# Optimization experiments

Measured on AMD Instinct MI355X. Metric: run time of the kernel, lower is better.

The kernel has to match this reference:

```python
import jax, jax.numpy as jnp
import numpy as np

B, S, C, H = 2, 3144, 256, 8
HD = C // H                      # head_dim = key_dim = 32
SCALE = HD ** -0.5
QN = 8                           # queriesNum hard-coded in source
KS = 5                           # lepe depthwise conv kernel


def setup_inputs() -> dict:
    key = jax.random.key(0)
    ks = jax.random.split(key, 10)
    gain_qkv = 2 ** (-2.5) * (2.0 / (C + C)) ** 0.5  # xavier_normal std with gain 2^-2.5
    gain_out = (2.0 / (C + C)) ** 0.5
    return {
        "x": jax.random.normal(ks[0], (B, S, C), jnp.float32),
        "mask": jax.random.uniform(ks[1], (B, S, S), jnp.float32),
        "wq": jax.random.normal(ks[2], (C, C), jnp.float32) * gain_qkv,
        "bq": jnp.zeros((C,), jnp.float32),
        "wk": jax.random.normal(ks[3], (C, C), jnp.float32) * gain_qkv,
        "bk": jnp.zeros((C,), jnp.float32),
        "wv": jax.random.normal(ks[4], (C, C), jnp.float32) * gain_qkv,
        "bv": jnp.zeros((C,), jnp.float32),
        "lepe_w": jax.random.normal(ks[5], (KS, KS, 1, C), jnp.float32) * 0.05,  # depthwise HWIO
        "lepe_b": jnp.zeros((C,), jnp.float32),
        "wo": jax.random.normal(ks[6], (C, C), jnp.float32) * gain_out,
        "bo": jnp.zeros((C,), jnp.float32),
        "h": 56,
        "w": 56,
    }


def _dwconv(x_nhwc, kern, bias):
    # depthwise 5x5, stride 1, padding 2 (groups = channels)
    y = jax.lax.conv_general_dilated(
        x_nhwc, kern, window_strides=(1, 1), padding=((2, 2), (2, 2)),
        dimension_numbers=("NHWC", "HWIO", "NHWC"),
        feature_group_count=x_nhwc.shape[-1])
    return y + bias


def reference(x, mask, wq, bq, wk, bk, wv, bv, lepe_w, lepe_b, wo, bo, h, w):
    b, s, c = x.shape
    q = x @ wq.T + bq
    k = (x @ wk.T + bk) * SCALE
    v = x @ wv.T + bv
    # lepe positional residual on the non-query tokens
    lepe = _dwconv(v[:, QN:].reshape(b, h, w, c), lepe_w, lepe_b).reshape(b, h * w, c)
    qh = q.reshape(b, s, H, HD).transpose(0, 2, 1, 3)   # (b, H, s, hd)
    kh = k.reshape(b, s, H, HD).transpose(0, 2, 1, 3)
    vh = kh  # faithful to source: v_h = k.reshape(...)  (scaled k used as values)
    qk = jnp.einsum("bhqd,bhkd->bhqk", qh, kh)
    qk = qk + jnp.log(mask[:, None] + 1e-6)              # isSoftMask=True path
    attn = jax.nn.softmax(qk, axis=-1)
    out = jnp.einsum("bhqk,bhkd->bhqd", attn, vh)
    out = out.transpose(0, 2, 1, 3).reshape(b, s, c)
    out = out.at[:, QN:].add(lepe)
    return out @ wo.T + bo
```

## Files before the change

### kernel.cpp

```cpp
#include <hip/hip_runtime.h>


#define S_LEN 3144
#define SP    3200
#define HEADS 8
#define HD    32
#define BATCH 2
#define MROWS (BATCH*S_LEN)
#define NPIX  3136
#define SCALE_F 0.17677669529663687f
#define KQ_SC   0.25504472665352026f

typedef __bf16 bf16x8  __attribute__((ext_vector_type(8)));
typedef __bf16 bf16x4  __attribute__((ext_vector_type(4)));
typedef float  floatx4 __attribute__((ext_vector_type(4)));
typedef short  shortx4 __attribute__((ext_vector_type(4)));
typedef _Float16 halfx4 __attribute__((ext_vector_type(4)));
typedef _Float16 halfx8 __attribute__((ext_vector_type(8)));

static __device__ __forceinline__ float bf2f(unsigned int h) {
  union { unsigned int u; float f; } v; v.u = h << 16; return v.f;
}
static __device__ __forceinline__ unsigned short f2bf(float f) {
  union { __bf16 b; unsigned short u; } v; v.b = (__bf16)f; return v.u;
}
static __device__ __forceinline__ bf16x8 ldcvt8(const float* __restrict__ p) {
  float4 a = *(const float4*)p;
  float4 b = *(const float4*)(p + 4);
  bf16x8 r;
  r[0]=(__bf16)a.x; r[1]=(__bf16)a.y; r[2]=(__bf16)a.z; r[3]=(__bf16)a.w;
  r[4]=(__bf16)b.x; r[5]=(__bf16)b.y; r[6]=(__bf16)b.z; r[7]=(__bf16)b.w;
  return r;
}

#define GLOBAL_AS __attribute__((address_space(1)))
#define LDS_AS    __attribute__((address_space(3)))
static __device__ __forceinline__ void gload_lds16(const void* g, void* l) {
  __builtin_amdgcn_global_load_lds((const GLOBAL_AS void*)g, (LDS_AS void*)l, 16, 0, 0);
}

#define FENCE4() asm volatile("s_waitcnt vmcnt(4)" ::: "memory")
#define FENCE2() asm volatile("s_waitcnt vmcnt(2)" ::: "memory")
#define FENCE0() asm volatile("s_waitcnt vmcnt(0)" ::: "memory")

__global__ __launch_bounds__(256) void k_cvt(
    const float* __restrict__ x, const float* __restrict__ wq,
    const float* __restrict__ wk, const float* __restrict__ wv,
    unsigned short* __restrict__ xb, unsigned short* __restrict__ w3b)
{
  const int i = blockIdx.x * 256 + threadIdx.x;
  const int NX = MROWS * 32;
  const int NW = 8192;
  const float* src;
  unsigned short* dst;
  if (i < NX) { src = x + (size_t)i * 8; dst = xb + (size_t)i * 8; }
  else {
    const int j = i - NX;
    if (j >= 3 * NW) return;
    src = (j < NW) ? wq + (size_t)j * 8
        : (j < 2 * NW) ? wk + (size_t)(j - NW) * 8
                       : wv + (size_t)(j - 2 * NW) * 8;
    dst = w3b + (size_t)j * 8;
  }
  bf16x8 v = ldcvt8(src);
  *(bf16x8*)dst = v;
}

__global__ __launch_bounds__(256) void k_qkv_mp(
    const unsigned short* __restrict__ xb, const unsigned short* __restrict__ w3b,
    const float* __restrict__ bqp, const float* __restrict__ bkp,
    const float* __restrict__ bvp,
    unsigned short* __restrict__ qws, unsigned short* __restrict__ kws,
    unsigned short* __restrict__ vfrag, unsigned short* __restrict__ vstage,
    const float* __restrict__ mask, _Float16* __restrict__ pm)
{
  __shared__ unsigned short lds_t[64 * 65];
  const int blk = blockIdx.x;

  if (blk >= 1200) {
    const int mp = blk - 1200;
    const int bs = mp % 400;
    const int by = mp / 400;
    const int b  = bs / 200, strip = bs % 200;
    const int t  = threadIdx.x;
    const int n  = t & 127;
    const int tsel = t >> 7;
    const int row = n >> 3;
    const int k2  = n & 7;
    const int g0  = (2 * k2) ^ (row & 15);
    const int gbase = g0 & ~1;
    const bool swp = (g0 & 1);

    int mr = strip * 16 + row; if (mr >= S_LEN) mr = S_LEN - 1;
    const float* src = mask + ((size_t)b * S_LEN + mr) * S_LEN;
    _Float16* dst0 = pm + ((size_t)bs * 50) * 1024 + n * 8;

#pragma unroll 1
    for (int tt = 0; tt < 5; ++tt) {
      const int tile = by * 10 + tt * 2 + tsel;
      const int c0 = tile * 64 + gbase * 4;
      float4 a = make_float4(-1e-6f, -1e-6f, -1e-6f, -1e-6f);
      float4 c = a;
      if (c0 < S_LEN) {
        a = *(const float4*)(src + c0);
        c = *(const float4*)(src + c0 + 4);
      }
      const float4 fst = swp ? c : a;
      const float4 snd = swp ? a : c;
      halfx8 o;
      o[0] = (_Float16)(fst.x + 1e-6f); o[1] = (_Float16)(fst.y + 1e-6f);
      o[2] = (_Float16)(fst.z + 1e-6f); o[3] = (_Float16)(fst.w + 1e-6f);
      o[4] = (_Float16)(snd.x + 1e-6f); o[5] = (_Float16)(snd.y + 1e-6f);
      o[6] = (_Float16)(snd.z + 1e-6f); o[7] = (_Float16)(snd.w + 1e-6f);
      *(halfx8*)(dst0 + (size_t)tile * 1024) = o;
    }
    return;
  }

  const int xi = blk % 100;
  const int yi = blk / 100;
  const int lane = threadIdx.x & 63;
  const int wid  = threadIdx.x >> 6;
  const int c    = lane & 15, quad = lane >> 4;
  const int bsel  = xi / 50;
  const int stile = xi % 50;
  const int srow0 = stile * 64;
  const int ncol = yi * 64;
  const int wsel = ncol >> 8;
  const int col0 = ncol & 255;

  const float* bptr = (wsel == 0) ? bqp : (wsel == 1) ? bkp : bvp;

  const int srow = srow0 + wid * 16 + c;
  const int arow = bsel * S_LEN + ((srow < S_LEN) ? srow : 0);
  const unsigned short* ap = xb  + (size_t)arow * 256 + quad * 8;
  const unsigned short* bp = w3b + (size_t)(ncol + c) * 256 + quad * 8;

  floatx4 acc[4];
#pragma unroll
  for (int ct = 0; ct < 4; ++ct) acc[ct] = (floatx4){0.f, 0.f, 0.f, 0.f};

#pragma unroll
  for (int ks = 0; ks < 8; ++ks) {
    bf16x8 af = *(const bf16x8*)(ap + ks * 32);
#pragma unroll
    for (int ct = 0; ct < 4; ++ct) {
      bf16x8 bf = *(const bf16x8*)(bp + (size_t)ct * 16 * 256 + ks * 32);
      acc[ct] = __builtin_amdgcn_mfma_f32_16x16x32_bf16(af, bf, acc[ct], 0, 0, 0);
    }
  }

#pragma unroll
  for (int ct = 0; ct < 4; ++ct) {
    const int col = col0 + ct * 16 + c;
    const float bias = bptr[col];
#pragma unroll
    for (int r = 0; r < 4; ++r) {
      const int s = srow0 + wid * 16 + quad * 4 + r;
      const int valid = (s < S_LEN);
      const float v = acc[ct][r] + bias;
      if (wsel == 0) {
        qws[(((size_t)(bsel * HEADS + (col >> 5))) * SP + s) * HD + (col & 31)] =
            valid ? f2bf(v) : (unsigned short)0;
      } else if (wsel == 1) {
        kws[(((size_t)(bsel * HEADS + (col >> 5))) * SP + s) * HD + (col & 31)] =
            valid ? f2bf(v * KQ_SC) : (unsigned short)0;
        lds_t[(ct * 16 + c) * 65 + (wid * 16 + quad * 4 + r)] =
            valid ? f2bf(v * SCALE_F) : (unsigned short)0;
      } else {
        if (valid) vstage[(size_t)(bsel * S_LEN + s) * 256 + col] = f2bf(v);
      }
    }
  }

  if (wsel == 1) {
    __syncthreads();
    const int tid = threadIdx.x;
#pragma unroll
    for (int j = 0; j < 4; ++j) {
      const int grp  = j * 4 + (tid >> 6);
      const int l    = tid & 63;
      const int ct2  = grp & 3;
      const int half = (grp >> 2) & 1;
      const int hsel = grp >> 3;
      const int cc = l & 15, qq = l >> 4;
      const int cl = hsel * 32 + half * 16 + cc;
      const int rb = ct2 * 16 + qq * 4;
      union { shortx4 s4; unsigned short u[4]; } pk;
#pragma unroll
      for (int e = 0; e < 4; ++e) pk.u[e] = lds_t[cl * 65 + rb + e];
      const int hglob = (col0 >> 5) + hsel;
      const size_t off =
          ((((size_t)(bsel * HEADS + hglob) * 50 + stile) * 4 + ct2) * 2 + half) * 64 + l;
      *(shortx4*)(vfrag + off * 4) = pk.s4;
    }
  }
}

static __device__ void lepe_block(int idx,
                                  const unsigned short* __restrict__ vws,
                                  const float* __restrict__ cw,
                                  const float* __restrict__ cb,
                                  unsigned short* __restrict__ lepe)
{
  if (idx >= BATCH * NPIX * 32) return;
  const int cg = idx & 31;
  const int p  = (idx >> 5) % NPIX;
  const int b  = idx / (NPIX * 32);
  const int y  = p / 56, xx = p - y * 56;

  float acc[8];
  {
    float4 b0 = *(const float4*)(cb + cg * 8);
    float4 b1 = *(const float4*)(cb + cg * 8 + 4);
    acc[0]=b0.x; acc[1]=b0.y; acc[2]=b0.z; acc[3]=b0.w;
    acc[4]=b1.x; acc[5]=b1.y; acc[6]=b1.z; acc[7]=b1.w;
  }
#pragma unroll
  for (int dy = -2; dy <= 2; ++dy) {
    const int yy = y + dy;
    if ((unsigned)yy >= 56u) continue;
#pragma unroll
    for (int dx = -2; dx <= 2; ++dx) {
      const int xs = xx + dx;
      if ((unsigned)xs >= 56u) continue;
      uint4 vv = *(const uint4*)(vws + (size_t)(b * S_LEN + 8 + yy * 56 + xs) * 256 + cg * 8);
      const float* wp = cw + (size_t)((dy + 2) * 5 + (dx + 2)) * 256 + cg * 8;
      float4 w0 = *(const float4*)wp;
      float4 w1 = *(const float4*)(wp + 4);
      unsigned int va[4] = {vv.x, vv.y, vv.z, vv.w};
      acc[0] += bf2f(va[0] & 0xFFFFu) * w0.x;  acc[1] += bf2f(va[0] >> 16) * w0.y;
      acc[2] += bf2f(va[1] & 0xFFFFu) * w0.z;  acc[3] += bf2f(va[1] >> 16) * w0.w;
      acc[4] += bf2f(va[2] & 0xFFFFu) * w1.x;  acc[5] += bf2f(va[2] >> 16) * w1.y;
      acc[6] += bf2f(va[3] & 0xFFFFu) * w1.z;  acc[7] += bf2f(va[3] >> 16) * w1.w;
    }
  }
  unsigned int o[4];
#pragma unroll
  for (int j = 0; j < 4; ++j)
    o[j] = (unsigned int)f2bf(acc[2*j]) | ((unsigned int)f2bf(acc[2*j+1]) << 16);
  *((uint4*)(lepe + (size_t)(b * NPIX + p) * 256 + cg * 8)) = make_uint4(o[0], o[1], o[2], o[3]);
}

static __device__ __forceinline__ void proc_tile_pre(
    int t, const unsigned short* __restrict__ kb,
    const unsigned short* __restrict__ vb,
    const _Float16* __restrict__ mb,
    int c, int quad, int lane, const bf16x8 qf,
    floatx4& o0, floatx4& o1, float& l_run)
{
  const int k0 = t * 64;
  bf16x8 kf[4]; shortx4 v0[4], v1[4];
  const unsigned short* tb = vb + (size_t)t * 2048;
#pragma unroll
  for (int ct = 0; ct < 4; ++ct) {
    kf[ct] = *(const bf16x8*)(kb + (size_t)(k0 + ct * 16 + c) * HD + quad * 8);
    v0[ct] = *(const shortx4*)(tb + (ct * 2 + 0) * 256 + lane * 4);
    v1[ct] = *(const shortx4*)(tb + (ct * 2 + 1) * 256 + lane * 4);
  }
  floatx4 s[4];
#pragma unroll
  for (int ct = 0; ct < 4; ++ct)
    s[ct] = __builtin_amdgcn_mfma_f32_16x16x32_bf16(kf[ct], qf,
               (floatx4){0.f,0.f,0.f,0.f}, 0, 0, 0);
  float ls = 0.f;
  shortx4 pf[4];
#pragma unroll
  for (int ct = 0; ct < 4; ++ct) {
    const halfx4 mv = *(const halfx4*)(mb + c * 64 + (((ct * 4 + quad) ^ c) * 4));
    float pr[4];
    pr[0] = (float)mv[0] * __builtin_amdgcn_exp2f(s[ct][0]);
    pr[1] = (float)mv[1] * __builtin_amdgcn_exp2f(s[ct][1]);
    pr[2] = (float)mv[2] * __builtin_amdgcn_exp2f(s[ct][2]);
    pr[3] = (float)mv[3] * __builtin_amdgcn_exp2f(s[ct][3]);
    ls += (pr[0] + pr[1]) + (pr[2] + pr[3]);
    union { bf16x4 b4; shortx4 s4; } u;
    u.b4[0]=(__bf16)pr[0]; u.b4[1]=(__bf16)pr[1]; u.b4[2]=(__bf16)pr[2]; u.b4[3]=(__bf16)pr[3];
    pf[ct] = u.s4;
  }
  l_run += ls;
#pragma unroll
  for (int ct = 0; ct < 4; ++ct) {
    o0 = __builtin_amdgcn_mfma_f32_16x16x16bf16_1k(v0[ct], pf[ct], o0, 0, 0, 0);
    o1 = __builtin_amdgcn_mfma_f32_16x16x16bf16_1k(v1[ct], pf[ct], o1, 0, 0, 0);
  }
}

static __device__ __forceinline__ void stage_pre(
    const _Float16* __restrict__ mp_t, int lane, _Float16* dst)
{
#pragma unroll
  for (int i = 0; i < 2; ++i)
    gload_lds16(mp_t + i * 512 + lane * 8, dst + i * 512);
}

__global__ __launch_bounds__(256) void k_flash_lepe(
    const unsigned short* __restrict__ qws,
    const unsigned short* __restrict__ kws,
    const unsigned short* __restrict__ vfrag,
    const _Float16* __restrict__ pmask,
    const unsigned short* __restrict__ vws,
    const float* __restrict__ cw, const float* __restrict__ cb,
    unsigned short* __restrict__ lepe_out,
    float* __restrict__ atbf)
{
  __shared__ __align__(16) float smem[4][1024];
  if (blockIdx.x >= 3200) {
    lepe_block((blockIdx.x - 3200) * 256 + threadIdx.x, vws, cw, cb, lepe_out);
    return;
  }
  const int lane = threadIdx.x & 63;
  const int wid  = threadIdx.x >> 6;
  const int c    = lane & 15, quad = lane >> 4;
  const int u    = blockIdx.x;
  const int xcd  = u & 7;
  const int slot = u >> 3;
  const int h    = slot & 7;
  const int p    = (slot >> 3) * 8 + xcd;
  const int b    = p / 200;
  const int strip = p - b * 200;
  const int qrow = strip * 16 + c;
  const size_t bh = (size_t)(b * HEADS + h);

  const bf16x8 qf = *(const bf16x8*)(qws + (bh * SP + qrow) * HD + quad * 8);
  const unsigned short* kb = kws + bh * SP * HD;
  const unsigned short* vb = vfrag + bh * (size_t)(50 * 2048);
  const _Float16* mpb = pmask + (size_t)(b * 200 + strip) * (50 * 1024);
  _Float16* mt = (_Float16*)&smem[wid][0];

  float l_run = 0.f;
  floatx4 o0 = (floatx4){0.f,0.f,0.f,0.f};
  floatx4 o1 = (floatx4){0.f,0.f,0.f,0.f};

  const int tbase = wid * 12;
  const int nt = (wid < 2) ? 13 : 12;

  stage_pre(mpb + tbase * 1024, lane, mt);

  for (int it = 0; it < nt; ++it) {
    const int t = (it < 12) ? tbase + it : 48 + wid;
    if (it + 1 < nt) {
      const int tn = (it + 1 < 12) ? tbase + it + 1 : 48 + wid;
      stage_pre(mpb + tn * 1024, lane, mt + ((it + 1) & 1) * 1024);
      FENCE2();
    } else {
      FENCE0();
    }
    proc_tile_pre(t, kb, vb, mt + (it & 1) * 1024, c, quad, lane, qf, o0, o1, l_run);
  }

#pragma unroll
  for (int r = 0; r < 4; ++r) {
    smem[wid][lane * 9 + r]     = o0[r];
    smem[wid][lane * 9 + 4 + r] = o1[r];
  }
  smem[wid][lane * 9 + 8] = l_run;
  __syncthreads();

  if (wid == 0) {
#pragma unroll
    for (int w = 1; w < 4; ++w) {
#pragma unroll
      for (int r = 0; r < 4; ++r) {
        o0[r] += smem[w][lane * 9 + r];
        o1[r] += smem[w][lane * 9 + 4 + r];
      }
      l_run += smem[w][lane * 9 + 8];
    }
    l_run += __shfl_xor(l_run, 16);
    l_run += __shfl_xor(l_run, 32);
    const float rl = 1.f / l_run;

    if (qrow < S_LEN) {
      float* op = atbf + ((size_t)b * S_LEN + qrow) * 256 + h * 32;
      float4 s0 = make_float4(o0[0]*rl, o0[1]*rl, o0[2]*rl, o0[3]*rl);
      float4 s1 = make_float4(o1[0]*rl, o1[1]*rl, o1[2]*rl, o1[3]*rl);
      *(float4*)(op + quad * 4)      = s0;
      *(float4*)(op + 16 + quad * 4) = s1;
    }
  }
}

__global__ __launch_bounds__(256) void k_oproj(
    const float* __restrict__ atbf,
    const unsigned short* __restrict__ lepe,
    const float* __restrict__ wop,
    const float* __restrict__ bop,
    float* __restrict__ out)
{
  const int lane = threadIdx.x & 63;
  const int wid  = threadIdx.x >> 6;
  const int c = lane & 15, quad = lane >> 4;
  const int row0 = blockIdx.x * 64 + wid * 16;
  const int col0 = blockIdx.y * 32;

  int arow = row0 + c; if (arow >= MROWS) arow = 0;
  const int bb = (arow >= S_LEN) ? 1 : 0;
  const int sr = arow - bb * S_LEN;
  const bool hasl = (sr >= 8);
  const float* ap = atbf + (size_t)arow * 256 + quad * 8;
  const unsigned short* lp =
      lepe + (hasl ? (((size_t)bb * NPIX + (sr - 8)) * 256 + quad * 8) : 0);
  const float* bp = wop + (size_t)(col0 + c) * 256 + quad * 8;

  floatx4 acc[2];
#pragma unroll
  for (int ct = 0; ct < 2; ++ct) acc[ct] = (floatx4){0.f,0.f,0.f,0.f};
#pragma unroll
  for (int ks = 0; ks < 8; ++ks) {
    float4 a0 = *(const float4*)(ap + ks * 32);
    float4 a1 = *(const float4*)(ap + ks * 32 + 4);
    if (hasl) {
      uint4 lv = *(const uint4*)(lp + ks * 32);
      a0.x += bf2f(lv.x & 0xFFFFu); a0.y += bf2f(lv.x >> 16);
      a0.z += bf2f(lv.y & 0xFFFFu); a0.w += bf2f(lv.y >> 16);
      a1.x += bf2f(lv.z & 0xFFFFu); a1.y += bf2f(lv.z >> 16);
      a1.z += bf2f(lv.w & 0xFFFFu); a1.w += bf2f(lv.w >> 16);
    }
    bf16x8 af;
    af[0]=(__bf16)a0.x; af[1]=(__bf16)a0.y; af[2]=(__bf16)a0.z; af[3]=(__bf16)a0.w;
    af[4]=(__bf16)a1.x; af[5]=(__bf16)a1.y; af[6]=(__bf16)a1.z; af[7]=(__bf16)a1.w;
#pragma unroll
    for (int ct = 0; ct < 2; ++ct) {
      bf16x8 bf = ldcvt8(bp + (size_t)ct * 16 * 256 + ks * 32);
      acc[ct] = __builtin_amdgcn_mfma_f32_16x16x32_bf16(af, bf, acc[ct], 0, 0, 0);
    }
  }
#pragma unroll
  for (int ct = 0; ct < 2; ++ct) {
    const int col = col0 + ct * 16 + c;
    const float bias = bop[col];
#pragma unroll
    for (int r = 0; r < 4; ++r) {
      const int row = row0 + quad * 4 + r;
      if (row >= MROWS) continue;
      out[(size_t)row * 256 + col] = acc[ct][r] + bias;
    }
  }
}

__global__ __launch_bounds__(256) void k_lepe_sa(const unsigned short* __restrict__ vws,
                                                 const float* __restrict__ cw,
                                                 const float* __restrict__ cb,
                                                 unsigned short* __restrict__ lepe)
{
  lepe_block(blockIdx.x * 256 + threadIdx.x, vws, cw, cb, lepe);
}

template<bool TAIL>
static __device__ __forceinline__ void proc_tile_fb(
    int t, const unsigned short* __restrict__ kb,
    const unsigned short* __restrict__ vb,
    const float* __restrict__ mb,
    int c, int quad, int lane, const bf16x8 qf,
    floatx4& o0, floatx4& o1, float& l_run)
{
  const int k0 = t * 64;
  bf16x8 kf[4]; shortx4 v0[4], v1[4];
  const unsigned short* tb = vb + (size_t)t * 2048;
#pragma unroll
  for (int ct = 0; ct < 4; ++ct) {
    kf[ct] = *(const bf16x8*)(kb + (size_t)(k0 + ct * 16 + c) * HD + quad * 8);
    v0[ct] = *(const shortx4*)(tb + (ct * 2 + 0) * 256 + lane * 4);
    v1[ct] = *(const shortx4*)(tb + (ct * 2 + 1) * 256 + lane * 4);
  }
  floatx4 s[4];
#pragma unroll
  for (int ct = 0; ct < 4; ++ct)
    s[ct] = __builtin_amdgcn_mfma_f32_16x16x32_bf16(kf[ct], qf,
               (floatx4){0.f,0.f,0.f,0.f}, 0, 0, 0);
  float ls = 0.f;
  shortx4 pf[4];
#pragma unroll
  for (int ct = 0; ct < 4; ++ct) {
    const float4 mv = *(const float4*)(mb + c * 64 + (((ct * 4 + quad) ^ c) * 4));
    float pr[4];
    pr[0] = (mv.x + 1e-6f) * __builtin_amdgcn_exp2f(s[ct][0]);
    pr[1] = (mv.y + 1e-6f) * __builtin_amdgcn_exp2f(s[ct][1]);
    pr[2] = (mv.z + 1e-6f) * __builtin_amdgcn_exp2f(s[ct][2]);
    pr[3] = (mv.w + 1e-6f) * __builtin_amdgcn_exp2f(s[ct][3]);
    if (TAIL) {
      const int kk = k0 + ct * 16 + quad * 4;
#pragma unroll
      for (int r = 0; r < 4; ++r) if (kk + r >= S_LEN) pr[r] = 0.f;
    }
    ls += (pr[0] + pr[1]) + (pr[2] + pr[3]);
    union { bf16x4 b4; shortx4 s4; } u;
    u.b4[0]=(__bf16)pr[0]; u.b4[1]=(__bf16)pr[1]; u.b4[2]=(__bf16)pr[2]; u.b4[3]=(__bf16)pr[3];
    pf[ct] = u.s4;
  }
  l_run += ls;
#pragma unroll
  for (int ct = 0; ct < 4; ++ct) {
    o0 = __builtin_amdgcn_mfma_f32_16x16x16bf16_1k(v0[ct], pf[ct], o0, 0, 0, 0);
    o1 = __builtin_amdgcn_mfma_f32_16x16x16bf16_1k(v1[ct], pf[ct], o1, 0, 0, 0);
  }
}

static __device__ __forceinline__ void stage_mask_fb(
    const float* const (&msrc)[4], const int (&goff4)[4], int k0, float* dst)
{
#pragma unroll
  for (int i = 0; i < 4; ++i)
    gload_lds16(msrc[i] + (k0 + goff4[i]), dst + i * 256);
}

static __device__ __forceinline__ void stage_mask_tail_fb(
    const float* const (&msrc)[4], const int (&goff4)[4], int k0, float* dst)
{
#pragma unroll
  for (int i = 0; i < 4; ++i) {
    int kk = k0 + goff4[i];
    if (kk > S_LEN - 4) kk = S_LEN - 4;
    gload_lds16(msrc[i] + kk, dst + i * 256);
  }
}

__global__ __launch_bounds__(512) void k_flash_fb(
    const unsigned short* __restrict__ qws,
    const unsigned short* __restrict__ kws,
    const unsigned short* __restrict__ vfrag,
    const float* __restrict__ mask,
    float* __restrict__ atbf)
{
  __shared__ __align__(16) float smem[8][2048];
  const int lane = threadIdx.x & 63;
  const int wid  = threadIdx.x >> 6;
  const int c    = lane & 15, quad = lane >> 4;
  const int u    = blockIdx.x;
  const int xcd  = u & 7;
  const int slot = u >> 3;
  const int h    = slot & 7;
  const int p    = (slot >> 3) * 8 + xcd;
  const int b    = p / 200;
  const int strip = p - b * 200;
  const int qrow = strip * 16 + c;
  const size_t bh = (size_t)(b * HEADS + h);

  const bf16x8 qf = *(const bf16x8*)(qws + (bh * SP + qrow) * HD + quad * 8);
  const unsigned short* kb = kws + bh * SP * HD;
  const unsigned short* vb = vfrag + bh * (size_t)(50 * 2048);
  float* mt = &smem[wid][0];

  const float* msrc[4];
  int goff4[4];
#pragma unroll
  for (int i = 0; i < 4; ++i) {
    const int rq = i * 4 + (lane >> 4);
    int mr = strip * 16 + rq; if (mr >= S_LEN) mr = S_LEN - 1;
    msrc[i] = mask + ((size_t)b * S_LEN + mr) * S_LEN;
    goff4[i] = ((lane & 15) ^ rq) * 4;
  }

  float l_run = 0.f;
  floatx4 o0 = (floatx4){0.f,0.f,0.f,0.f};
  floatx4 o1 = (floatx4){0.f,0.f,0.f,0.f};

  const int tbase = wid * 6;
  const int nt = (wid < 2) ? 7 : 6;

  stage_mask_fb(msrc, goff4, tbase * 64, mt);

  for (int it = 0; it < nt; ++it) {
    const int t = (it < 6) ? tbase + it : 48 + wid;
    if (it + 1 < nt) {
      const int tn = (it + 1 < 6) ? tbase + it + 1 : 48 + wid;
      float* dst = mt + ((it + 1) & 1) * 1024;
      if (tn == 49) stage_mask_tail_fb(msrc, goff4, 49 * 64, dst);
      else          stage_mask_fb(msrc, goff4, tn * 64, dst);
      FENCE4();
    } else {
      FENCE0();
    }
    const float* mb = mt + (it & 1) * 1024;
    if (wid == 1 && it == 6)
      proc_tile_fb<true >(t, kb, vb, mb, c, quad, lane, qf, o0, o1, l_run);
    else
      proc_tile_fb<false>(t, kb, vb, mb, c, quad, lane, qf, o0, o1, l_run);
  }

#pragma unroll
  for (int r = 0; r < 4; ++r) {
    smem[wid][lane * 9 + r]     = o0[r];
    smem[wid][lane * 9 + 4 + r] = o1[r];
  }
  smem[wid][lane * 9 + 8] = l_run;
  __syncthreads();

  if (wid == 0) {
#pragma unroll
    for (int w = 1; w < 8; ++w) {
#pragma unroll
      for (int r = 0; r < 4; ++r) {
        o0[r] += smem[w][lane * 9 + r];
        o1[r] += smem[w][lane * 9 + 4 + r];
      }
      l_run += smem[w][lane * 9 + 8];
    }
    l_run += __shfl_xor(l_run, 16);
    l_run += __shfl_xor(l_run, 32);
    const float rl = 1.f / l_run;

    if (qrow < S_LEN) {
      float* op = atbf + ((size_t)b * S_LEN + qrow) * 256 + h * 32;
      float4 s0 = make_float4(o0[0]*rl, o0[1]*rl, o0[2]*rl, o0[3]*rl);
      float4 s1 = make_float4(o1[0]*rl, o1[1]*rl, o1[2]*rl, o1[3]*rl);
      *(float4*)(op + quad * 4)      = s0;
      *(float4*)(op + 16 + quad * 4) = s1;
    }
  }
}

#define QW_OFF 0u
#define KW_OFF 3276800u
#define VF_OFF 6553600u
#define LE_OFF 9830400u
#define AT_OFF 13041664u
#define PM_OFF 19480576u
#define PM_NEED (19480576u + 40960000u)

extern "C" void kernel_launch(void* const* d_in, const int* in_sizes, int n_in,
                              void* d_out, int out_size, void* d_ws, size_t ws_size,
                              hipStream_t stream) {
  const float* x    = (const float*)d_in[0];
  const float* mask = (const float*)d_in[1];
  const float* wq   = (const float*)d_in[2];
  const float* bq   = (const float*)d_in[3];
  const float* wk   = (const float*)d_in[4];
  const float* bk   = (const float*)d_in[5];
  const float* wv   = (const float*)d_in[6];
  const float* bv   = (const float*)d_in[7];
  const float* lw   = (const float*)d_in[8];
  const float* lb   = (const float*)d_in[9];
  const float* wo   = (const float*)d_in[10];
  const float* bo   = (const float*)d_in[11];

  char* ws = (char*)d_ws;
  unsigned short* qws = (unsigned short*)(ws + QW_OFF);
  unsigned short* kws = (unsigned short*)(ws + KW_OFF);
  unsigned short* vfr = (unsigned short*)(ws + VF_OFF);
  unsigned short* w3b = (unsigned short*)(ws + LE_OFF);
  unsigned short* lpe = (unsigned short*)(ws + LE_OFF);
  float*          atf = (float*)(ws + AT_OFF);
  unsigned short* vst = (unsigned short*)d_out;
  unsigned short* xb  = (unsigned short*)d_out + 1609728;
  float*          outf = (float*)d_out;

  const bool use_pre = (ws_size >= (size_t)PM_NEED);

  k_cvt<<<882, 256, 0, stream>>>(x, wq, wk, wv, xb, w3b);
  if (use_pre) {
    _Float16* pm = (_Float16*)(ws + PM_OFF);
    k_qkv_mp<<<3200, 256, 0, stream>>>(xb, w3b, bq, bk, bv, qws, kws, vfr, vst, mask, pm);
    k_flash_lepe<<<3984, 256, 0, stream>>>(qws, kws, vfr, pm, vst, lw, lb, lpe, atf);
  } else {
    k_qkv_mp<<<1200, 256, 0, stream>>>(xb, w3b, bq, bk, bv, qws, kws, vfr, vst,
                                       mask, (_Float16*)nullptr);
    k_lepe_sa<<<784, 256, 0, stream>>>(vst, lw, lb, lpe);
    k_flash_fb<<<3200, 512, 0, stream>>>(qws, kws, vfr, mask, atf);
  }
  k_oproj<<<dim3(99, 8), 256, 0, stream>>>(atf, lpe, wo, bo, outf);
}
```

Before: 295.8 us.

## Fuse x bf16 conversion into QKV projection and pre-convert output weights

Drops the separate conversion of x to bf16: the QKV projection now loads fp32 x, converts it into LDS per 16-row tile, and each block computes all 768 output columns, with its four waves splitting them. The weight conversion kernel now also converts wo to bf16, so the output projection reads bf16 weights instead of converting fp32 per load. Block decomposition for QKV changes from 64x64 tiles to 16-row full-width strips, and the V-fragment transpose is redone for the new tiling. This removes one full pass over x and its bf16 staging, at the cost of fewer, larger QKV blocks and more repeated reads of the QKV weights.

```diff
diff --git a/kernel.cpp b/kernel.cpp
--- a/kernel.cpp
+++ b/kernel.cpp
@@ -43,42 +43,38 @@
 #define FENCE2() asm volatile("s_waitcnt vmcnt(2)" ::: "memory")
 #define FENCE0() asm volatile("s_waitcnt vmcnt(0)" ::: "memory")
 
-__global__ __launch_bounds__(256) void k_cvt(
-    const float* __restrict__ x, const float* __restrict__ wq,
-    const float* __restrict__ wk, const float* __restrict__ wv,
-    unsigned short* __restrict__ xb, unsigned short* __restrict__ w3b)
+__global__ __launch_bounds__(256) void k_cvtw(
+    const float* __restrict__ wq, const float* __restrict__ wk,
+    const float* __restrict__ wv, const float* __restrict__ wo,
+    unsigned short* __restrict__ w3b, unsigned short* __restrict__ wob)
 {
   const int i = blockIdx.x * 256 + threadIdx.x;
-  const int NX = MROWS * 32;
   const int NW = 8192;
-  const float* src;
-  unsigned short* dst;
-  if (i < NX) { src = x + (size_t)i * 8; dst = xb + (size_t)i * 8; }
-  else {
-    const int j = i - NX;
-    if (j >= 3 * NW) return;
-    src = (j < NW) ? wq + (size_t)j * 8
-        : (j < 2 * NW) ? wk + (size_t)(j - NW) * 8
-                       : wv + (size_t)(j - 2 * NW) * 8;
-    dst = w3b + (size_t)j * 8;
-  }
-  bf16x8 v = ldcvt8(src);
-  *(bf16x8*)dst = v;
+  if (i < 3 * NW) {
+    const float* src = (i < NW) ? wq + (size_t)i * 8
+                     : (i < 2 * NW) ? wk + (size_t)(i - NW) * 8
+                                    : wv + (size_t)(i - 2 * NW) * 8;
+    *(bf16x8*)(w3b + (size_t)i * 8) = ldcvt8(src);
+  } else if (i < 4 * NW) {
+    const int j = i - 3 * NW;
+    *(bf16x8*)(wob + (size_t)j * 8) = ldcvt8(wo + (size_t)j * 8);
+  }
 }
 
 __global__ __launch_bounds__(256) void k_qkv_mp(
-    const unsigned short* __restrict__ xb, const unsigned short* __restrict__ w3b,
+    const float* __restrict__ x, const unsigned short* __restrict__ w3b,
     const float* __restrict__ bqp, const float* __restrict__ bkp,
     const float* __restrict__ bvp,
     unsigned short* __restrict__ qws, unsigned short* __restrict__ kws,
     unsigned short* __restrict__ vfrag, unsigned short* __restrict__ vstage,
     const float* __restrict__ mask, _Float16* __restrict__ pm)
 {
-  __shared__ unsigned short lds_t[64 * 65];
+  __shared__ __align__(16) unsigned short lds_a[16][264];
+  __shared__ __align__(16) unsigned short lds_k[256][17];
   const int blk = blockIdx.x;
 
-  if (blk >= 1200) {
-    const int mp = blk - 1200;
+  if (blk >= 400) {
+    const int mp = blk - 400;
     const int bs = mp % 400;
     const int by = mp / 400;
     const int b  = bs / 200, strip = bs % 200;
@@ -117,83 +113,84 @@
     return;
   }
 
-  const int xi = blk % 100;
-  const int yi = blk / 100;
-  const int lane = threadIdx.x & 63;
-  const int wid  = threadIdx.x >> 6;
+  const int bsel = blk / 200;
+  const int b16  = blk % 200;
+  const int srow0 = b16 * 16;
+  const int tid  = threadIdx.x;
+  const int lane = tid & 63;
+  const int wid  = tid >> 6;
   const int c    = lane & 15, quad = lane >> 4;
-  const int bsel  = xi / 50;
-  const int stile = xi % 50;
-  const int srow0 = stile * 64;
-  const int ncol = yi * 64;
-  const int wsel = ncol >> 8;
-  const int col0 = ncol & 255;
-
-  const float* bptr = (wsel == 0) ? bqp : (wsel == 1) ? bkp : bvp;
-
-  const int srow = srow0 + wid * 16 + c;
-  const int arow = bsel * S_LEN + ((srow < S_LEN) ? srow : 0);
-  const unsigned short* ap = xb  + (size_t)arow * 256 + quad * 8;
-  const unsigned short* bp = w3b + (size_t)(ncol + c) * 256 + quad * 8;
-
-  floatx4 acc[4];
-#pragma unroll
-  for (int ct = 0; ct < 4; ++ct) acc[ct] = (floatx4){0.f, 0.f, 0.f, 0.f};
-
-#pragma unroll
-  for (int ks = 0; ks < 8; ++ks) {
-    bf16x8 af = *(const bf16x8*)(ap + ks * 32);
-#pragma unroll
-    for (int ct = 0; ct < 4; ++ct) {
-      bf16x8 bf = *(const bf16x8*)(bp + (size_t)ct * 16 * 256 + ks * 32);
-      acc[ct] = __builtin_amdgcn_mfma_f32_16x16x32_bf16(af, bf, acc[ct], 0, 0, 0);
-    }
-  }
-
-#pragma unroll
-  for (int ct = 0; ct < 4; ++ct) {
-    const int col = col0 + ct * 16 + c;
+
+  {
+    const int row = tid >> 4;
+    const int seg = tid & 15;
+    const int s   = srow0 + row;
+    if (s < S_LEN) {
+      const float* xp = x + ((size_t)bsel * S_LEN + s) * 256 + seg * 16;
+      *(bf16x8*)&lds_a[row][seg * 16]     = ldcvt8(xp);
+      *(bf16x8*)&lds_a[row][seg * 16 + 8] = ldcvt8(xp + 8);
+    } else {
+      bf16x8 z = {};
+      *(bf16x8*)&lds_a[row][seg * 16]     = z;
+      *(bf16x8*)&lds_a[row][seg * 16 + 8] = z;
+    }
+  }
+  __syncthreads();
+
+  bf16x8 af[8];
+#pragma unroll
+  for (int ks = 0; ks < 8; ++ks)
+    af[ks] = *(const bf16x8*)&lds_a[c][ks * 32 + quad * 8];
+
+#pragma unroll 1
+  for (int j = 0; j < 12; ++j) {
+    const int gcol = wid * 192 + j * 16;
+    const int wsel = gcol >> 8;
+    const int col0 = gcol & 255;
+    const unsigned short* bp = w3b + (size_t)(gcol + c) * 256 + quad * 8;
+
+    floatx4 acc = (floatx4){0.f, 0.f, 0.f, 0.f};
+#pragma unroll
+    for (int ks = 0; ks < 8; ++ks) {
+      bf16x8 bf = *(const bf16x8*)(bp + ks * 32);
+      acc = __builtin_amdgcn_mfma_f32_16x16x32_bf16(af[ks], bf, acc, 0, 0, 0);
+    }
+
+    const float* bptr = (wsel == 0) ? bqp : (wsel == 1) ? bkp : bvp;
+    const int col = col0 + c;
     const float bias = bptr[col];
 #pragma unroll
     for (int r = 0; r < 4; ++r) {
-      const int s = srow0 + wid * 16 + quad * 4 + r;
+      const int s = srow0 + quad * 4 + r;
       const int valid = (s < S_LEN);
-      const float v = acc[ct][r] + bias;
+      const float v = acc[r] + bias;
       if (wsel == 0) {
         qws[(((size_t)(bsel * HEADS + (col >> 5))) * SP + s) * HD + (col & 31)] =
             valid ? f2bf(v) : (unsigned short)0;
       } else if (wsel == 1) {
         kws[(((size_t)(bsel * HEADS + (col >> 5))) * SP + s) * HD + (col & 31)] =
             valid ? f2bf(v * KQ_SC) : (unsigned short)0;
-        lds_t[(ct * 16 + c) * 65 + (wid * 16 + quad * 4 + r)] =
-            valid ? f2bf(v * SCALE_F) : (unsigned short)0;
+        lds_k[col][quad * 4 + r] = valid ? f2bf(v * SCALE_F) : (unsigned short)0;
       } else {
         if (valid) vstage[(size_t)(bsel * S_LEN + s) * 256 + col] = f2bf(v);
       }
     }
   }
-
-  if (wsel == 1) {
-    __syncthreads();
-    const int tid = threadIdx.x;
-#pragma unroll
-    for (int j = 0; j < 4; ++j) {
-      const int grp  = j * 4 + (tid >> 6);
-      const int l    = tid & 63;
-      const int ct2  = grp & 3;
-      const int half = (grp >> 2) & 1;
-      const int hsel = grp >> 3;
-      const int cc = l & 15, qq = l >> 4;
-      const int cl = hsel * 32 + half * 16 + cc;
-      const int rb = ct2 * 16 + qq * 4;
-      union { shortx4 s4; unsigned short u[4]; } pk;
-#pragma unroll
-      for (int e = 0; e < 4; ++e) pk.u[e] = lds_t[cl * 65 + rb + e];
-      const int hglob = (col0 >> 5) + hsel;
-      const size_t off =
-          ((((size_t)(bsel * HEADS + hglob) * 50 + stile) * 4 + ct2) * 2 + half) * 64 + l;
-      *(shortx4*)(vfrag + off * 4) = pk.s4;
-    }
+  __syncthreads();
+
+  const int stile = b16 >> 2, ct2 = b16 & 3;
+#pragma unroll
+  for (int jj = 0; jj < 4; ++jj) {
+    const int u = (tid >> 6) + jj * 4;
+    const int h = u >> 1, half = u & 1;
+    const int l = tid & 63;
+    union { shortx4 s4; unsigned short us[4]; } pk;
+#pragma unroll
+    for (int e = 0; e < 4; ++e)
+      pk.us[e] = lds_k[h * 32 + half * 16 + (l & 15)][(l >> 4) * 4 + e];
+    const size_t off =
+        ((((size_t)(bsel * HEADS + h) * 50 + stile) * 4 + ct2) * 2 + half) * 64 + l;
+    *(shortx4*)(vfrag + off * 4) = pk.s4;
   }
 }
 
@@ -384,7 +381,7 @@
 __global__ __launch_bounds__(256) void k_oproj(
     const float* __restrict__ atbf,
     const unsigned short* __restrict__ lepe,
-    const float* __restrict__ wop,
+    const unsigned short* __restrict__ wob,
     const float* __restrict__ bop,
     float* __restrict__ out)
 {
@@ -401,7 +398,7 @@
   const float* ap = atbf + (size_t)arow * 256 + quad * 8;
   const unsigned short* lp =
       lepe + (hasl ? (((size_t)bb * NPIX + (sr - 8)) * 256 + quad * 8) : 0);
-  const float* bp = wop + (size_t)(col0 + c) * 256 + quad * 8;
+  const unsigned short* bp = wob + (size_t)(col0 + c) * 256 + quad * 8;
 
   floatx4 acc[2];
 #pragma unroll
@@ -422,7 +419,7 @@
     af[4]=(__bf16)a1.x; af[5]=(__bf16)a1.y; af[6]=(__bf16)a1.z; af[7]=(__bf16)a1.w;
 #pragma unroll
     for (int ct = 0; ct < 2; ++ct) {
-      bf16x8 bf = ldcvt8(bp + (size_t)ct * 16 * 256 + ks * 32);
+      bf16x8 bf = *(const bf16x8*)(bp + (size_t)ct * 16 * 256 + ks * 32);
       acc[ct] = __builtin_amdgcn_mfma_f32_16x16x32_bf16(af, bf, acc[ct], 0, 0, 0);
     }
   }
@@ -616,8 +613,10 @@
 #define VF_OFF 6553600u
 #define LE_OFF 9830400u
 #define AT_OFF 13041664u
-#define PM_OFF 19480576u
-#define PM_NEED (19480576u + 40960000u)
+#define WB_OFF 19480576u
+#define WO_OFF 19873792u
+#define PM_OFF 20004864u
+#define PM_NEED (20004864u + 40960000u)
 
 extern "C" void kernel_launch(void* const* d_in, const int* in_sizes, int n_in,
                               void* d_out, int out_size, void* d_ws, size_t ws_size,
@@ -639,25 +638,25 @@
   unsigned short* qws = (unsigned short*)(ws + QW_OFF);
   unsigned short* kws = (unsigned short*)(ws + KW_OFF);
   unsigned short* vfr = (unsigned short*)(ws + VF_OFF);
-  unsigned short* w3b = (unsigned short*)(ws + LE_OFF);
   unsigned short* lpe = (unsigned short*)(ws + LE_OFF);
   float*          atf = (float*)(ws + AT_OFF);
+  unsigned short* w3b = (unsigned short*)(ws + WB_OFF);
+  unsigned short* wob = (unsigned short*)(ws + WO_OFF);
   unsigned short* vst = (unsigned short*)d_out;
-  unsigned short* xb  = (unsigned short*)d_out + 1609728;
   float*          outf = (float*)d_out;
 
   const bool use_pre = (ws_size >= (size_t)PM_NEED);
 
-  k_cvt<<<882, 256, 0, stream>>>(x, wq, wk, wv, xb, w3b);
+  k_cvtw<<<128, 256, 0, stream>>>(wq, wk, wv, wo, w3b, wob);
   if (use_pre) {
     _Float16* pm = (_Float16*)(ws + PM_OFF);
-    k_qkv_mp<<<3200, 256, 0, stream>>>(xb, w3b, bq, bk, bv, qws, kws, vfr, vst, mask, pm);
+    k_qkv_mp<<<2400, 256, 0, stream>>>(x, w3b, bq, bk, bv, qws, kws, vfr, vst, mask, pm);
     k_flash_lepe<<<3984, 256, 0, stream>>>(qws, kws, vfr, pm, vst, lw, lb, lpe, atf);
   } else {
-    k_qkv_mp<<<1200, 256, 0, stream>>>(xb, w3b, bq, bk, bv, qws, kws, vfr, vst,
-                                       mask, (_Float16*)nullptr);
+    k_qkv_mp<<<400, 256, 0, stream>>>(x, w3b, bq, bk, bv, qws, kws, vfr, vst,
+                                      mask, (_Float16*)nullptr);
     k_lepe_sa<<<784, 256, 0, stream>>>(vst, lw, lb, lpe);
     k_flash_fb<<<3200, 512, 0, stream>>>(qws, kws, vfr, mask, atf);
   }
-  k_oproj<<<dim3(99, 8), 256, 0, stream>>>(atf, lpe, wo, bo, outf);
-}
+  k_oproj<<<dim3(99, 8), 256, 0, stream>>>(atf, lpe, wob, bo, outf);
+}
```

Result: faster. 282.5 us (-4.5%).
